# Performance work log

Measured on AMD Instinct MI355X. Metric: run time of the kernel, lower is better.

Reference implementation:

```python
import jax, jax.numpy as jnp
import numpy as np

B, N, D, KG, L = 4, 256, 256, 128, 2
EPS = 1e-5


def setup_inputs() -> dict:
    key = jax.random.key(0)
    ks = jax.random.split(key, 8)
    s = 0.05  # weight init scale
    return {
        "node_feats": jax.random.normal(ks[0], (B, N, D), dtype=jnp.float32),
        "kg_relation_embeddings": jax.random.normal(ks[1], (B, N, N, KG), dtype=jnp.float32),
        "kg_adjacency": jax.random.randint(ks[2], (B, N, N), 0, 2, dtype=jnp.int32),
        # kg_proj: Linear(kg_embed_dim -> node_dim)
        "W_kg": (jax.random.normal(ks[3], (KG, D), dtype=jnp.float32) * s),
        "b_kg": jnp.zeros((D,), dtype=jnp.float32),
        # per-layer MLP: Linear(3D -> D), ReLU, Linear(D -> D); stacked over L layers
        "W1": (jax.random.normal(ks[4], (L, 3 * D, D), dtype=jnp.float32) * s),
        "b1": jnp.zeros((L, D), dtype=jnp.float32),
        "W2": (jax.random.normal(ks[5], (L, D, D), dtype=jnp.float32) * s),
        "b2": jnp.zeros((L, D), dtype=jnp.float32),
        # shared LayerNorm(node_dim)
        "gamma": jnp.ones((D,), dtype=jnp.float32),
        "beta": jnp.zeros((D,), dtype=jnp.float32),
    }


def _layer_norm(x, gamma, beta):
    mu = x.mean(-1, keepdims=True)
    var = ((x - mu) ** 2).mean(-1, keepdims=True)
    return (x - mu) * jax.lax.rsqrt(var + EPS) * gamma + beta


def reference(node_feats, kg_relation_embeddings, kg_adjacency,
              W_kg, b_kg, W1, b1, W2, b2, gamma, beta):
    d = node_feats.shape[-1]
    n_layers = W1.shape[0]
    # kg_proj applied to relation embeddings (same every layer; dropout is eval-mode identity)
    rel_proj = kg_relation_embeddings @ W_kg + b_kg            # (B,N,N,D)
    adj = kg_adjacency[..., None].astype(node_feats.dtype)     # (B,N,N,1)
    h = node_feats
    for l in range(n_layers):
        # split first Linear over the concat [hi, hj, rel_proj] -> avoids building (B,N,N,3D)
        Wa, Wb, Wc = W1[l, :d], W1[l, d:2 * d], W1[l, 2 * d:]
        a = h @ Wa                                             # (B,N,D) contribution of hi
        b = h @ Wb                                             # (B,N,D) contribution of hj
        c = jnp.einsum('bijk,kd->bijd', rel_proj, Wc)          # (B,N,N,D)
        pre = a[:, :, None, :] + b[:, None, :, :] + c + b1[l]  # (B,N,N,D)
        m = jax.nn.relu(pre) @ W2[l] + b2[l]                   # (B,N,N,D)
        msg = (m * adj).sum(axis=2)                            # (B,N,D) sum over source nodes j
        h = _layer_norm(h + msg, gamma, beta)
    return h
```

## Files before the change

### kernel.cpp

```cpp
#include <hip/hip_runtime.h>
#include <hip/hip_bf16.h>

#define B_ 4
#define N_ 256
#define D_ 256
#define KG_ 128
#define EPS_ 1e-5f

typedef __bf16 bf16x8 __attribute__((ext_vector_type(8)));
typedef __bf16 bf16x4 __attribute__((ext_vector_type(4)));
typedef float  f32x4v __attribute__((ext_vector_type(4)));

__device__ __forceinline__ void gload16(const void* g, void* l) {
    __builtin_amdgcn_global_load_lds(
        (const __attribute__((address_space(1))) uint32_t*)g,
        (__attribute__((address_space(3))) uint32_t*)l, 16, 0, 0);
}

__global__ __launch_bounds__(256) void s1_kernel(
    const float* __restrict__ Wkg, const float* __restrict__ W1l,
    const float* __restrict__ bkg, const float* __restrict__ b1l,
    __bf16* __restrict__ WkcT, float* __restrict__ biastot)
{
    const int d = threadIdx.x;
    if (blockIdx.x == KG_) {
        float acc = 0.f;
        for (int k = 0; k < D_; ++k)
            acc += bkg[k] * W1l[(2 * D_ + k) * D_ + d];
        biastot[d] = acc + b1l[d];
        return;
    }
    const int g = blockIdx.x;
    float acc = 0.f;
    for (int k = 0; k < D_; ++k)
        acc += Wkg[g * D_ + k] * W1l[(2 * D_ + k) * D_ + d];
    WkcT[d * KG_ + g] = (__bf16)acc;
}

__global__ __launch_bounds__(256) void s2_kernel(
    const float* __restrict__ hin, const float* __restrict__ W1l,
    const float* __restrict__ biastot,
    float* __restrict__ apb, __bf16* __restrict__ bbout)
{
    __shared__ float hT[D_][4];
    const int tid = threadIdx.x;
    const int R = blockIdx.x * 4;
    {
        const int r = tid & 3, c4 = (tid >> 2) << 2;
        const float4 v = *(const float4*)(hin + (R + r) * D_ + c4);
        hT[c4 + 0][r] = v.x; hT[c4 + 1][r] = v.y;
        hT[c4 + 2][r] = v.z; hT[c4 + 3][r] = v.w;
    }
    __syncthreads();
    float aa[4] = {0.f, 0.f, 0.f, 0.f};
    float ab[4] = {0.f, 0.f, 0.f, 0.f};
#pragma unroll 4
    for (int e = 0; e < D_; ++e) {
        const float wa = W1l[e * D_ + tid];
        const float wb = W1l[(D_ + e) * D_ + tid];
        const float4 hv = *(const float4*)&hT[e][0];
        aa[0] += hv.x * wa; aa[1] += hv.y * wa; aa[2] += hv.z * wa; aa[3] += hv.w * wa;
        ab[0] += hv.x * wb; ab[1] += hv.y * wb; ab[2] += hv.z * wb; ab[3] += hv.w * wb;
    }
    const float bt = biastot[tid];
#pragma unroll
    for (int r = 0; r < 4; ++r) {
        apb[(R + r) * D_ + tid]    = aa[r] + bt;
        bbout[(R + r) * D_ + tid]  = (__bf16)ab[r];
    }
}

template<int FROMB>
__global__ __launch_bounds__(256) void big_kernel(
    const float* __restrict__ rel, __bf16* __restrict__ relb,
    const int* __restrict__ adj,
    const __bf16* __restrict__ WkcT, const float* __restrict__ apb,
    const __bf16* __restrict__ bb, const float* __restrict__ W2l,
    const float* __restrict__ b2l, const float* __restrict__ hin,
    const float* __restrict__ gmm, const float* __restrict__ bta,
    float* __restrict__ hout)
{
    __shared__ __align__(16) __bf16 Et[N_ * KG_];
    __shared__ float adjL[N_];
    __shared__ float rL[D_];
    __shared__ float red[8];
    __shared__ float sdeg;

    const int tid = threadIdx.x;
    const int lane = tid & 63;
    const int w = tid >> 6;
    const int l15 = lane & 15;
    const int lg = lane >> 4;
    const int bi = blockIdx.x;
    const int dw = w * 64;

    const float*  Ebase  = rel + (size_t)bi * N_ * KG_;
    const __bf16* bbBase = bb + (size_t)(bi >> 8) * N_ * D_;

    bf16x8 wf[4][4];
#pragma unroll
    for (int nb = 0; nb < 4; ++nb)
#pragma unroll
        for (int kk = 0; kk < 4; ++kk)
            wf[nb][kk] = *(const bf16x8*)(WkcT + (dw + nb * 16 + l15) * KG_ + kk * 32 + lg * 8);

    f32x4v apbv[4];
#pragma unroll
    for (int nb = 0; nb < 4; ++nb)
        apbv[nb] = *(const f32x4v*)(apb + bi * D_ + dw + nb * 16 + lg * 4);

    adjL[tid] = (float)adj[bi * N_ + tid];

    if (FROMB) {
        const char* Gb = (const char*)(relb + (size_t)bi * N_ * KG_);
        char* ldsw = (char*)Et + (tid & 192) * 16;
#pragma unroll
        for (int i = 0; i < 16; ++i) {
            const int u = tid + i * 256;
            const int gu = (u & ~15) | ((u & 15) ^ ((u >> 4) & 7));
            gload16(Gb + gu * 16, ldsw + i * 4096);
        }
    } else {
        __bf16* relbW = relb ? relb + (size_t)bi * N_ * KG_ : nullptr;
#pragma unroll
        for (int rep = 0; rep < 16; ++rep) {
            const int v = tid + rep * 256;
            const int row = v >> 4;
            const int k0 = (v & 15) * 8;
            const float* s = Ebase + row * KG_ + k0;
            const f32x4v fa = *(const f32x4v*)s;
            const f32x4v fb = *(const f32x4v*)(s + 4);
            bf16x8 v8;
            v8[0] = (__bf16)fa[0]; v8[1] = (__bf16)fa[1];
            v8[2] = (__bf16)fa[2]; v8[3] = (__bf16)fa[3];
            v8[4] = (__bf16)fb[0]; v8[5] = (__bf16)fb[1];
            v8[6] = (__bf16)fb[2]; v8[7] = (__bf16)fb[3];
            const int off = (row * 256 + k0 * 2) ^ ((row & 7) << 4);
            *(bf16x8*)((char*)Et + off) = v8;
            if (relbW) *(bf16x8*)(relbW + v * 8) = v8;
        }
    }
    __syncthreads();

    float racc[4][4] = {};

#pragma unroll 4
    for (int jj = 0; jj < 16; ++jj) {
        const int row = jj * 16 + l15;
        bf16x8 af[4];
#pragma unroll
        for (int kk = 0; kk < 4; ++kk) {
            const int off = (row * 256 + kk * 64 + lg * 16) ^ ((row & 7) << 4);
            af[kk] = *(const bf16x8*)((const char*)Et + off);
        }
        f32x4v acc[4];
#pragma unroll
        for (int nb = 0; nb < 4; ++nb) acc[nb] = (f32x4v){0.f, 0.f, 0.f, 0.f};
#pragma unroll
        for (int kk = 0; kk < 4; ++kk)
#pragma unroll
            for (int nb = 0; nb < 4; ++nb)
                acc[nb] = __builtin_amdgcn_mfma_f32_16x16x32_bf16(wf[nb][kk], af[kk], acc[nb], 0, 0, 0);

        const float adjj = adjL[row];
        const __bf16* brow = bbBase + row * D_ + dw + lg * 4;
#pragma unroll
        for (int nb = 0; nb < 4; ++nb) {
            const bf16x4 bv = *(const bf16x4*)(brow + nb * 16);
#pragma unroll
            for (int q = 0; q < 4; ++q) {
                float t = acc[nb][q] + apbv[nb][q] + (float)bv[q];
                t = fmaxf(t, 0.f);
                racc[nb][q] += t * adjj;
            }
        }
    }

#pragma unroll
    for (int nb = 0; nb < 4; ++nb) {
        float v0 = racc[nb][0], v1 = racc[nb][1], v2 = racc[nb][2], v3 = racc[nb][3];
#pragma unroll
        for (int off = 1; off <= 8; off <<= 1) {
            v0 += __shfl_xor(v0, off, 64);
            v1 += __shfl_xor(v1, off, 64);
            v2 += __shfl_xor(v2, off, 64);
            v3 += __shfl_xor(v3, off, 64);
        }
        if (l15 == 0) {
            float4 o; o.x = v0; o.y = v1; o.z = v2; o.w = v3;
            *(float4*)&rL[dw + nb * 16 + lg * 4] = o;
        }
    }
    if (w == 0) {
        float s = adjL[lane] + adjL[lane + 64] + adjL[lane + 128] + adjL[lane + 192];
#pragma unroll
        for (int off = 32; off >= 1; off >>= 1) s += __shfl_xor(s, off, 64);
        if (lane == 0) sdeg = s;
    }
    __syncthreads();

    const int d = tid;
    float m0 = 0.f, m1 = 0.f, m2 = 0.f, m3 = 0.f;
#pragma unroll 8
    for (int e = 0; e < D_; e += 4) {
        const float4 rv = *(const float4*)&rL[e];
        m0 += rv.x * W2l[(e + 0) * D_ + d];
        m1 += rv.y * W2l[(e + 1) * D_ + d];
        m2 += rv.z * W2l[(e + 2) * D_ + d];
        m3 += rv.w * W2l[(e + 3) * D_ + d];
    }
    const float t = hin[bi * D_ + d] + (m0 + m1) + (m2 + m3) + sdeg * b2l[d];

    float s = t, sq = t * t;
#pragma unroll
    for (int off = 32; off >= 1; off >>= 1) {
        s  += __shfl_xor(s, off, 64);
        sq += __shfl_xor(sq, off, 64);
    }
    if (lane == 0) { red[w] = s; red[4 + w] = sq; }
    __syncthreads();
    const float S  = red[0] + red[1] + red[2] + red[3];
    const float SQ = red[4] + red[5] + red[6] + red[7];
    const float mu = S * (1.f / D_);
    const float var = SQ * (1.f / D_) - mu * mu;
    const float rstd = rsqrtf(var + EPS_);
    hout[bi * D_ + d] = (t - mu) * rstd * gmm[d] + bta[d];
}

extern "C" void kernel_launch(void* const* d_in, const int* in_sizes, int n_in,
                              void* d_out, int out_size, void* d_ws, size_t ws_size,
                              hipStream_t stream)
{
    const float* node  = (const float*)d_in[0];
    const float* rel   = (const float*)d_in[1];
    const int*   adj   = (const int*)d_in[2];
    const float* Wkg   = (const float*)d_in[3];
    const float* bkg   = (const float*)d_in[4];
    const float* W1    = (const float*)d_in[5];
    const float* b1    = (const float*)d_in[6];
    const float* W2    = (const float*)d_in[7];
    const float* b2    = (const float*)d_in[8];
    const float* gamma = (const float*)d_in[9];
    const float* beta  = (const float*)d_in[10];
    float* out = (float*)d_out;

    char* ws = (char*)d_ws;
    float*  h1    = (float*)(ws);
    float*  apb   = (float*)(ws + (1 << 20));
    __bf16* bbuf  = (__bf16*)(ws + (2 << 20));
    float*  bias  = (float*)(ws + (3 << 20));
    __bf16* WkcT  = (__bf16*)(ws + (3 << 20) + 4096);
    __bf16* relb  = (__bf16*)(ws + (8 << 20));

    const size_t relElems = (size_t)B_ * N_ * N_ * KG_;
    const bool useBF = ws_size >= ((size_t)(8 << 20) + relElems * 2);
    __bf16* relbArg = useBF ? relb : nullptr;

    for (int l = 0; l < 2; ++l) {
        const float* W1l = W1 + (size_t)l * 3 * D_ * D_;
        const float* hin = (l == 0) ? node : h1;
        float* hout = (l == 1) ? out : h1;

        s1_kernel<<<KG_ + 1, 256, 0, stream>>>(Wkg, W1l, bkg, b1 + l * D_, WkcT, bias);
        s2_kernel<<<(B_ * N_) / 4, 256, 0, stream>>>(hin, W1l, bias, apb, bbuf);
        if (l == 0 || !useBF)
            big_kernel<0><<<B_ * N_, 256, 0, stream>>>(rel, relbArg, adj, WkcT, apb, bbuf,
                                                       W2 + (size_t)l * D_ * D_, b2 + l * D_,
                                                       hin, gamma, beta, hout);
        else
            big_kernel<1><<<B_ * N_, 256, 0, stream>>>(rel, relbArg, adj, WkcT, apb, bbuf,
                                                       W2 + (size_t)l * D_ * D_, b2 + l * D_,
                                                       hin, gamma, beta, hout);
    }
}
```

Baseline: 208.5 us.

## Split big kernel over source-node chunks and move W2/LayerNorm to tail kernel

Each (b,i) block now processes only a quarter of the source nodes j, so the grid grows fourfold and each block uses a quarter of the LDS. Each block writes its partial ReLU sums to a workspace buffer. A new tail kernel adds the four partials, computes the degree, applies W2 and the bias, and does the LayerNorm. This aims to raise occupancy and overlap of memory loads, at the cost of an extra launch and the per-block weight-fragment loads being repeated across four times as many blocks.

```diff
diff --git a/kernel.cpp b/kernel.cpp
--- a/kernel.cpp
+++ b/kernel.cpp
@@ -75,27 +75,24 @@
     const float* __restrict__ rel, __bf16* __restrict__ relb,
     const int* __restrict__ adj,
     const __bf16* __restrict__ WkcT, const float* __restrict__ apb,
-    const __bf16* __restrict__ bb, const float* __restrict__ W2l,
-    const float* __restrict__ b2l, const float* __restrict__ hin,
-    const float* __restrict__ gmm, const float* __restrict__ bta,
-    float* __restrict__ hout)
-{
-    __shared__ __align__(16) __bf16 Et[N_ * KG_];
-    __shared__ float adjL[N_];
-    __shared__ float rL[D_];
-    __shared__ float red[8];
-    __shared__ float sdeg;
+    const __bf16* __restrict__ bb, float* __restrict__ rbuf)
+{
+    __shared__ __align__(16) __bf16 Et[64 * KG_];
+    __shared__ float adjL[64];
 
     const int tid = threadIdx.x;
     const int lane = tid & 63;
     const int w = tid >> 6;
     const int l15 = lane & 15;
     const int lg = lane >> 4;
-    const int bi = blockIdx.x;
+    const int bij = blockIdx.x;
+    const int bi = bij >> 2;
+    const int jc = bij & 3;
+    const int j0 = jc * 64;
     const int dw = w * 64;
 
-    const float*  Ebase  = rel + (size_t)bi * N_ * KG_;
-    const __bf16* bbBase = bb + (size_t)(bi >> 8) * N_ * D_;
+    const float*  Ebase  = rel + ((size_t)bi * N_ + j0) * KG_;
+    const __bf16* bbBase = bb + (size_t)(bi >> 8) * N_ * D_ + j0 * D_;
 
     bf16x8 wf[4][4];
 #pragma unroll
@@ -109,21 +106,21 @@
     for (int nb = 0; nb < 4; ++nb)
         apbv[nb] = *(const f32x4v*)(apb + bi * D_ + dw + nb * 16 + lg * 4);
 
-    adjL[tid] = (float)adj[bi * N_ + tid];
+    if (tid < 64) adjL[tid] = (float)adj[bi * N_ + j0 + tid];
 
     if (FROMB) {
-        const char* Gb = (const char*)(relb + (size_t)bi * N_ * KG_);
+        const char* Gb = (const char*)(relb + ((size_t)bi * N_ + j0) * KG_);
         char* ldsw = (char*)Et + (tid & 192) * 16;
 #pragma unroll
-        for (int i = 0; i < 16; ++i) {
+        for (int i = 0; i < 4; ++i) {
             const int u = tid + i * 256;
             const int gu = (u & ~15) | ((u & 15) ^ ((u >> 4) & 7));
             gload16(Gb + gu * 16, ldsw + i * 4096);
         }
     } else {
-        __bf16* relbW = relb ? relb + (size_t)bi * N_ * KG_ : nullptr;
-#pragma unroll
-        for (int rep = 0; rep < 16; ++rep) {
+        __bf16* relbW = relb ? relb + ((size_t)bi * N_ + j0) * KG_ : nullptr;
+#pragma unroll
+        for (int rep = 0; rep < 4; ++rep) {
             const int v = tid + rep * 256;
             const int row = v >> 4;
             const int k0 = (v & 15) * 8;
@@ -144,8 +141,8 @@
 
     float racc[4][4] = {};
 
-#pragma unroll 4
-    for (int jj = 0; jj < 16; ++jj) {
+#pragma unroll
+    for (int jj = 0; jj < 4; ++jj) {
         const int row = jj * 16 + l15;
         bf16x8 af[4];
 #pragma unroll
@@ -176,6 +173,7 @@
         }
     }
 
+    float* rout = rbuf + (size_t)bij * D_;
 #pragma unroll
     for (int nb = 0; nb < 4; ++nb) {
         float v0 = racc[nb][0], v1 = racc[nb][1], v2 = racc[nb][2], v3 = racc[nb][3];
@@ -188,16 +186,35 @@
         }
         if (l15 == 0) {
             float4 o; o.x = v0; o.y = v1; o.z = v2; o.w = v3;
-            *(float4*)&rL[dw + nb * 16 + lg * 4] = o;
-        }
-    }
-    if (w == 0) {
-        float s = adjL[lane] + adjL[lane + 64] + adjL[lane + 128] + adjL[lane + 192];
-#pragma unroll
-        for (int off = 32; off >= 1; off >>= 1) s += __shfl_xor(s, off, 64);
-        if (lane == 0) sdeg = s;
-    }
-    __syncthreads();
+            *(float4*)(rout + dw + nb * 16 + lg * 4) = o;
+        }
+    }
+}
+
+__global__ __launch_bounds__(256) void tail_kernel(
+    const float* __restrict__ rbuf, const int* __restrict__ adj,
+    const float* __restrict__ W2l, const float* __restrict__ b2l,
+    const float* __restrict__ hin, const float* __restrict__ gmm,
+    const float* __restrict__ bta, float* __restrict__ hout)
+{
+    __shared__ float rL[D_];
+    __shared__ float red[8];
+    __shared__ float dred[4];
+
+    const int tid = threadIdx.x;
+    const int lane = tid & 63;
+    const int w = tid >> 6;
+    const int bi = blockIdx.x;
+
+    const float* rp = rbuf + (size_t)bi * 4 * D_;
+    rL[tid] = rp[tid] + rp[D_ + tid] + rp[2 * D_ + tid] + rp[3 * D_ + tid];
+
+    float a = (float)adj[bi * N_ + tid];
+#pragma unroll
+    for (int off = 32; off >= 1; off >>= 1) a += __shfl_xor(a, off, 64);
+    if (lane == 0) dred[w] = a;
+    __syncthreads();
+    const float sdeg = dred[0] + dred[1] + dred[2] + dred[3];
 
     const int d = tid;
     float m0 = 0.f, m1 = 0.f, m2 = 0.f, m3 = 0.f;
@@ -250,6 +267,7 @@
     __bf16* bbuf  = (__bf16*)(ws + (2 << 20));
     float*  bias  = (float*)(ws + (3 << 20));
     __bf16* WkcT  = (__bf16*)(ws + (3 << 20) + 4096);
+    float*  rbuf  = (float*)(ws + (4 << 20));
     __bf16* relb  = (__bf16*)(ws + (8 << 20));
 
     const size_t relElems = (size_t)B_ * N_ * N_ * KG_;
@@ -264,12 +282,10 @@
         s1_kernel<<<KG_ + 1, 256, 0, stream>>>(Wkg, W1l, bkg, b1 + l * D_, WkcT, bias);
         s2_kernel<<<(B_ * N_) / 4, 256, 0, stream>>>(hin, W1l, bias, apb, bbuf);
         if (l == 0 || !useBF)
-            big_kernel<0><<<B_ * N_, 256, 0, stream>>>(rel, relbArg, adj, WkcT, apb, bbuf,
-                                                       W2 + (size_t)l * D_ * D_, b2 + l * D_,
-                                                       hin, gamma, beta, hout);
+            big_kernel<0><<<B_ * N_ * 4, 256, 0, stream>>>(rel, relbArg, adj, WkcT, apb, bbuf, rbuf);
         else
-            big_kernel<1><<<B_ * N_, 256, 0, stream>>>(rel, relbArg, adj, WkcT, apb, bbuf,
-                                                       W2 + (size_t)l * D_ * D_, b2 + l * D_,
-                                                       hin, gamma, beta, hout);
-    }
-}
+            big_kernel<1><<<B_ * N_ * 4, 256, 0, stream>>>(rel, relbArg, adj, WkcT, apb, bbuf, rbuf);
+        tail_kernel<<<B_ * N_, 256, 0, stream>>>(rbuf, adj, W2 + (size_t)l * D_ * D_,
+                                                 b2 + l * D_, hin, gamma, beta, hout);
+    }
+}
```

After: 249.7 us. 1.2x slower.
